# Performance work log

Measured on AMD Instinct MI355X. Metric: run time of the kernel, lower is better.

Reference implementation:

```python
import jax, jax.numpy as jnp
import numpy as np

B, N, D, H = 2, 2048, 1024, 16
DH = D // H
MASK_VALUE = -1e7


def setup_inputs() -> dict:
    key = jax.random.key(0)
    ks = jax.random.split(key, 8)
    scale = 0.02
    return {
        "queries": jax.random.normal(ks[0], (B, N, D), dtype=jnp.float32),
        "keys": jax.random.normal(ks[1], (B, N, D), dtype=jnp.float32),
        "values": jax.random.normal(ks[2], (B, N, D), dtype=jnp.float32),
        "valid_len": jax.random.randint(ks[3], (B * H,), 1, N + 1, dtype=jnp.int32),
        "Wq": jax.random.normal(ks[4], (D, D), dtype=jnp.float32) * scale,
        "Wk": jax.random.normal(ks[5], (D, D), dtype=jnp.float32) * scale,
        "Wv": jax.random.normal(ks[6], (D, D), dtype=jnp.float32) * scale,
        "Wo": jax.random.normal(ks[7], (D, D), dtype=jnp.float32) * scale,
    }


def reference(queries, keys, values, valid_len, Wq, Wk, Wv, Wo):
    b, n, d = queries.shape
    h, dh = H, d // H

    def split_heads(x):  # (b, n, d) -> (b, h, n, dh)
        return x.reshape(b, n, h, dh).transpose(0, 2, 1, 3)

    q = split_heads(queries @ Wq)
    k = split_heads(keys @ Wk)
    v = split_heads(values @ Wv)

    # (b, h, nq, nk) full score tensor, as in the original naive bmm path
    scores = jnp.einsum("bhqd,bhkd->bhqk", q, k) / jnp.sqrt(jnp.float32(dh))

    # valid_len is 1-D of length b*h; repeat_interleave over queries means the
    # mask depends only on the key index: keep k < valid_len[bh]
    vl = valid_len.reshape(b, h, 1, 1)
    keep = jnp.arange(n)[None, None, None, :] < vl  # (b, h, 1, nk)
    scores = jnp.where(keep, scores, MASK_VALUE)

    attn = jax.nn.softmax(scores, axis=-1)
    heads = jnp.einsum("bhqk,bhkd->bhqd", attn, v)  # (b, h, n, dh)
    out = heads.transpose(0, 2, 1, 3).reshape(b, n, d) @ Wo
    return out
```

## Files before the change

### kernel.cpp

```cpp
#include <hip/hip_runtime.h>

#define B_ 2
#define N_ 2048
#define D_ 1024
#define H_ 16
#define DH_ 64
#define NITEMS 1024

typedef _Float16 half8 __attribute__((ext_vector_type(8)));
typedef _Float16 half4 __attribute__((ext_vector_type(4)));
typedef float f32x4 __attribute__((ext_vector_type(4)));

__device__ __forceinline__ void gl2lds16(const _Float16* g, _Float16* l) {
  __builtin_amdgcn_global_load_lds(
      (const __attribute__((address_space(1))) void*)g,
      (__attribute__((address_space(3))) void*)l, 16, 0, 0);
}

__global__ __launch_bounds__(256) void prep_kernel(
    const float* __restrict__ q, const float* __restrict__ k,
    const float* __restrict__ v, const float* __restrict__ Wq,
    const float* __restrict__ Wk, const float* __restrict__ Wv,
    const float* __restrict__ Wo, const int* __restrict__ vlen,
    _Float16* __restrict__ Xf, _Float16* __restrict__ WtAll,
    int* __restrict__ order) {
  __shared__ float tile[64][65];
  const int bid = blockIdx.x;
  if (bid < 6144) {
    int y = bid >> 11, x = bid & 2047;
    const float* s = (y == 0) ? q : (y == 1) ? k : v;
    _Float16* d = Xf + (size_t)y * ((size_t)B_ * N_ * D_);
    size_t idx = ((size_t)x * 256 + threadIdx.x) * 8;
    float4 a = *(const float4*)(s + idx);
    float4 b = *(const float4*)(s + idx + 4);
    half8 h;
    h[0] = (_Float16)a.x; h[1] = (_Float16)a.y; h[2] = (_Float16)a.z; h[3] = (_Float16)a.w;
    h[4] = (_Float16)b.x; h[5] = (_Float16)b.y; h[6] = (_Float16)b.z; h[7] = (_Float16)b.w;
    *(half8*)(d + idx) = h;
  } else if (bid < 6144 + 1024) {
    int idx = bid - 6144;
    int z = idx >> 8, rem = idx & 255, gy = rem >> 4, gx = rem & 15;
    const float* W = (z == 0) ? Wq : (z == 1) ? Wk : (z == 2) ? Wv : Wo;
    _Float16* Wt = WtAll + (size_t)z * D_ * D_;
    int k0 = gy * 64, n0 = gx * 64;
    int tr = threadIdx.x >> 4, tc = threadIdx.x & 15;
#pragma unroll
    for (int i = 0; i < 4; ++i) {
      int r = tr + i * 16;
      float4 va = *(const float4*)(W + (size_t)(k0 + r) * D_ + n0 + tc * 4);
      tile[r][tc * 4 + 0] = va.x; tile[r][tc * 4 + 1] = va.y;
      tile[r][tc * 4 + 2] = va.z; tile[r][tc * 4 + 3] = va.w;
    }
    __syncthreads();
#pragma unroll
    for (int i = 0; i < 4; ++i) {
      int r = tr + i * 16;
      half4 hv;
      hv[0] = (_Float16)tile[tc * 4 + 0][r];
      hv[1] = (_Float16)tile[tc * 4 + 1][r];
      hv[2] = (_Float16)tile[tc * 4 + 2][r];
      hv[3] = (_Float16)tile[tc * 4 + 3][r];
      *(half4*)(Wt + (size_t)(n0 + r) * D_ + k0 + tc * 4) = hv;
    }
  } else {
    int i = threadIdx.x;
    if (i < B_ * H_) {
      int vi = vlen[i], rank = 0;
      for (int j = 0; j < B_ * H_; ++j) {
        int vj = vlen[j];
        if (vj > vi || (vj == vi && j < i)) ++rank;
      }
      order[rank] = i;
    }
  }
}

#define BK 32

template <int NT, int MODE>
__global__ __launch_bounds__(256) void gemm_f16_kernel(
    const _Float16* __restrict__ Aall, const _Float16* __restrict__ Btall,
    _Float16* __restrict__ ChAll, float* __restrict__ Cf32) {
  constexpr int BN = NT * 32;
  constexpr int K = D_;
  __shared__ __attribute__((aligned(16))) _Float16 As[128 * BK];
  __shared__ __attribute__((aligned(16))) _Float16 Bs[BN * BK];
  const int z = blockIdx.z;
  const _Float16* A  = Aall  + (size_t)z * ((size_t)B_ * N_ * D_);
  const _Float16* Bt = Btall + (size_t)z * ((size_t)D_ * D_);
  _Float16* Chead = ChAll + (size_t)z * ((size_t)B_ * N_ * D_);

  const int tid = threadIdx.x;
  const int m0 = blockIdx.y * 128, n0 = blockIdx.x * BN;
  const int lane = tid & 63, w = tid >> 6;
  const int quad = lane >> 4, l15 = lane & 15;
  const int wm = (w >> 1) * 64, wn = (w & 1) * (BN / 2);
  const int swz = (quad ^ ((l15 >> 1) & 3)) * 8;
  f32x4 acc[4][NT] = {};

  for (int kt = 0; kt < K; kt += BK) {
    if (kt) __syncthreads();
#pragma unroll
    for (int p = 0; p < 2; ++p) {
      int c = p * 256 + tid;
      int row = c >> 2, pg = c & 3;
      int gl = pg ^ ((row >> 1) & 3);
      gl2lds16(A + (size_t)(m0 + row) * K + kt + gl * 8, &As[c * 8]);
    }
#pragma unroll
    for (int p = 0; p < NT / 2; ++p) {
      int c = p * 256 + tid;
      int row = c >> 2, pg = c & 3;
      int gl = pg ^ ((row >> 1) & 3);
      gl2lds16(Bt + (size_t)(n0 + row) * K + kt + gl * 8, &Bs[c * 8]);
    }
    __syncthreads();
    half8 af[4], bf[NT];
#pragma unroll
    for (int mt = 0; mt < 4; ++mt)
      af[mt] = *(const half8*)&As[(wm + mt * 16 + l15) * 32 + swz];
#pragma unroll
    for (int nt = 0; nt < NT; ++nt)
      bf[nt] = *(const half8*)&Bs[(wn + nt * 16 + l15) * 32 + swz];
#pragma unroll
    for (int mt = 0; mt < 4; ++mt)
#pragma unroll
      for (int nt = 0; nt < NT; ++nt)
        acc[mt][nt] = __builtin_amdgcn_mfma_f32_16x16x32_f16(
            af[mt], bf[nt], acc[mt][nt], 0, 0, 0);
  }

#pragma unroll
  for (int mt = 0; mt < 4; ++mt) {
    int mrow = m0 + wm + mt * 16 + quad * 4;
#pragma unroll
    for (int nt = 0; nt < NT; ++nt) {
      int jcol = n0 + wn + nt * 16 + l15;
      if (MODE == 0) {
        int b = mrow >> 11, n = mrow & (N_ - 1);
        int h = jcol >> 6, dh = jcol & (DH_ - 1);
        if (z == 2) {
          half4 o;
#pragma unroll
          for (int r = 0; r < 4; ++r) o[r] = (_Float16)acc[mt][nt][r];
          *(half4*)(ChAll + 2 * (size_t)B_ * N_ * D_ +
                    ((size_t)(b * H_ + h) * DH_ + dh) * N_ + n) = o;
        } else {
#pragma unroll
          for (int r = 0; r < 4; ++r)
            Chead[((((size_t)(b * H_ + h)) * N_ + n + r) * DH_) + dh] =
                (_Float16)acc[mt][nt][r];
        }
      } else {
#pragma unroll
        for (int r = 0; r < 4; ++r)
          Cf32[(size_t)(mrow + r) * D_ + jcol] = acc[mt][nt][r];
      }
    }
  }
}

__global__ __launch_bounds__(256, 4) void attn_kernel(
    const _Float16* __restrict__ Qh, const _Float16* __restrict__ Kh,
    const _Float16* __restrict__ VtG, const int* __restrict__ vlen,
    _Float16* __restrict__ Hd, const int* __restrict__ order) {
  __shared__ __attribute__((aligned(16))) _Float16 Ks[2][64 * 64];
  __shared__ __attribute__((aligned(16))) _Float16 Vt[2][64 * 64];
  const int tid = threadIdx.x, lane = tid & 63, w = tid >> 6;
  const int quad = lane >> 4, l15 = lane & 15;
  const int sw  = (quad ^ (l15 & 7)) * 8;
  const int sw2 = ((quad + 4) ^ (l15 & 7)) * 8;
  const float sc2 = 0.125f * 1.44269504088896f;
  const half4 ones = {(_Float16)1, (_Float16)1, (_Float16)1, (_Float16)1};

  const int bid = blockIdx.x;
  const int item = (bid & 3) * 256 + (bid >> 2);
  const int bh = order[item >> 5];
  const int q0 = (item & 31) * 64;
  const int b = bh >> 4, h = bh & (H_ - 1);
  const int vl = vlen[bh];
  const int KT = (vl + 63) >> 6;
  const _Float16* Qb = Qh  + (size_t)bh * N_ * DH_;
  const _Float16* Kb = Kh  + (size_t)bh * N_ * DH_;
  const _Float16* Vb = VtG + (size_t)bh * N_ * DH_;

  const half8 qb0 = *(const half8*)(Qb + (size_t)(q0 + w * 16 + l15) * DH_ + quad * 8);
  const half8 qb1 = *(const half8*)(Qb + (size_t)(q0 + w * 16 + l15) * DH_ + 32 + quad * 8);

  half8 kpre[2], vpre[2];
  auto prefetch = [&](int k0k) {
#pragma unroll
    for (int p = 0; p < 2; ++p) {
      int c = p * 256 + tid;
      int row = c >> 3, pg = c & 7;
      kpre[p] = *(const half8*)(Kb + (size_t)(k0k + row) * DH_ + (pg ^ (row & 7)) * 8);
      vpre[p] = *(const half8*)(Vb + (size_t)row * N_ + k0k + pg * 8);
    }
  };
  auto commit = [&](int buf) {
#pragma unroll
    for (int p = 0; p < 2; ++p) {
      int c = p * 256 + tid;
      int row = c >> 3, pg = c & 7;
      *(half8*)&Ks[buf][c * 8] = kpre[p];
      int j0 = (pg * 2) ^ (row & 15), j1 = (pg * 2 + 1) ^ (row & 15);
      half4 lo = {vpre[p][0], vpre[p][1], vpre[p][2], vpre[p][3]};
      half4 hi = {vpre[p][4], vpre[p][5], vpre[p][6], vpre[p][7]};
      *(half4*)&Vt[buf][row * 64 + j0 * 4] = lo;
      *(half4*)&Vt[buf][row * 64 + j1 * 4] = hi;
    }
  };

  prefetch(0);
  commit(0);
  if (KT > 1) prefetch(64);
  __syncthreads();

  f32x4 Oacc[4] = {};
  f32x4 lacc = {};

  for (int kt = 0; kt < KT; ++kt) {
    const int cur = kt & 1;
    if (kt + 1 < KT) commit(1 - cur);
    if (kt + 2 < KT) prefetch((kt + 2) * 64);

    f32x4 s[4];
#pragma unroll
    for (int nt = 0; nt < 4; ++nt) {
      int r = nt * 16 + l15;
      half8 ka0 = *(const half8*)&Ks[cur][r * 64 + sw];
      half8 ka1 = *(const half8*)&Ks[cur][r * 64 + sw2];
      f32x4 c = {};
      c = __builtin_amdgcn_mfma_f32_16x16x32_f16(ka0, qb0, c, 0, 0, 0);
      c = __builtin_amdgcn_mfma_f32_16x16x32_f16(ka1, qb1, c, 0, 0, 0);
      s[nt] = c;
    }
    const int k0k = kt * 64;
    half4 pf[4];
    if (k0k + 64 <= vl) {
#pragma unroll
      for (int nt = 0; nt < 4; ++nt)
#pragma unroll
        for (int r = 0; r < 4; ++r)
          pf[nt][r] = (_Float16)exp2f(s[nt][r] * sc2);
    } else {
#pragma unroll
      for (int nt = 0; nt < 4; ++nt) {
        int keyb = k0k + nt * 16 + quad * 4;
#pragma unroll
        for (int r = 0; r < 4; ++r) {
          float p = exp2f(s[nt][r] * sc2);
          pf[nt][r] = (keyb + r < vl) ? (_Float16)p : (_Float16)0.f;
        }
      }
    }
#pragma unroll
    for (int nt = 0; nt < 4; ++nt) {
      lacc = __builtin_amdgcn_mfma_f32_16x16x16f16(ones, pf[nt], lacc, 0, 0, 0);
#pragma unroll
      for (int dt = 0; dt < 4; ++dt) {
        int dh = dt * 16 + l15;
        half4 va = *(const half4*)&Vt[cur][dh * 64 + (((nt * 4 + quad) ^ l15) << 2)];
        Oacc[dt] = __builtin_amdgcn_mfma_f32_16x16x16f16(va, pf[nt], Oacc[dt], 0, 0, 0);
      }
    }
    asm volatile("s_waitcnt lgkmcnt(0)" ::: "memory");
    __builtin_amdgcn_s_barrier();
    __builtin_amdgcn_sched_barrier(0);
  }

  float inv_l = 1.0f / lacc[0];
  int q = q0 + w * 16 + l15;
  _Float16* out = Hd + ((size_t)(b * N_ + q)) * D_ + h * DH_;
#pragma unroll
  for (int dt = 0; dt < 4; ++dt) {
    half4 o;
#pragma unroll
    for (int r = 0; r < 4; ++r) o[r] = (_Float16)(Oacc[dt][r] * inv_l);
    *(half4*)(out + dt * 16 + quad * 4) = o;
  }
}

extern "C" void kernel_launch(void* const* d_in, const int* in_sizes, int n_in,
                              void* d_out, int out_size, void* d_ws, size_t ws_size,
                              hipStream_t stream) {
  const float* q  = (const float*)d_in[0];
  const float* k  = (const float*)d_in[1];
  const float* v  = (const float*)d_in[2];
  const int*   vl = (const int*)d_in[3];
  const float* Wq = (const float*)d_in[4];
  const float* Wk = (const float*)d_in[5];
  const float* Wv = (const float*)d_in[6];
  const float* Wo = (const float*)d_in[7];

  const size_t XSZ = (size_t)B_ * N_ * D_;
  const size_t WSZ = (size_t)D_ * D_;
  _Float16* ws = (_Float16*)d_ws;
  _Float16* Xf = ws;
  _Float16* Wt = Xf + 3 * XSZ;
  _Float16* Qh = Wt + 4 * WSZ;
  _Float16* Hd = Qh + 3 * XSZ;
  int* order = (int*)(Hd + XSZ);

  prep_kernel<<<dim3(6144 + 1024 + 1), 256, 0, stream>>>(
      q, k, v, Wq, Wk, Wv, Wo, vl, Xf, Wt, order);

  gemm_f16_kernel<4, 0><<<dim3(D_ / 128, 32, 3), 256, 0, stream>>>(
      Xf, Wt, Qh, nullptr);

  attn_kernel<<<dim3(NITEMS), 256, 0, stream>>>(
      Qh, Qh + XSZ, Qh + 2 * XSZ, vl, Hd, order);

  gemm_f16_kernel<2, 1><<<dim3(D_ / 64, 32, 1), 256, 0, stream>>>(
      Hd, Wt + 3 * WSZ, nullptr, (float*)d_out);
}
```

Measured before the change: 236.4 us.

## Split attention keys across warps with register-direct K/V loads and LDS reduction

Restructures the attention kernel so each of the four warps handles all 64 queries but only a quarter of the key strips, reading K and V fragments straight from global memory into registers with a one-strip register prefetch. This removes the shared-memory staging of K/V tiles and the per-iteration block barriers. Partial O and row sums are then reduced across warps through LDS. It costs four times the accumulator registers, hence the lower occupancy hint, and uncoalesced scalar output stores. Block-index swizzling is also dropped.

```diff
diff --git a/kernel.cpp b/kernel.cpp
--- a/kernel.cpp
+++ b/kernel.cpp
@@ -160,124 +160,137 @@
   }
 }
 
-__global__ __launch_bounds__(256, 4) void attn_kernel(
+__global__ __launch_bounds__(256, 2) void attn_kernel(
     const _Float16* __restrict__ Qh, const _Float16* __restrict__ Kh,
     const _Float16* __restrict__ VtG, const int* __restrict__ vlen,
     _Float16* __restrict__ Hd, const int* __restrict__ order) {
-  __shared__ __attribute__((aligned(16))) _Float16 Ks[2][64 * 64];
-  __shared__ __attribute__((aligned(16))) _Float16 Vt[2][64 * 64];
+  __shared__ float Opart[2][64 * 65];
+  __shared__ float Lpart[2][64];
   const int tid = threadIdx.x, lane = tid & 63, w = tid >> 6;
   const int quad = lane >> 4, l15 = lane & 15;
-  const int sw  = (quad ^ (l15 & 7)) * 8;
-  const int sw2 = ((quad + 4) ^ (l15 & 7)) * 8;
   const float sc2 = 0.125f * 1.44269504088896f;
   const half4 ones = {(_Float16)1, (_Float16)1, (_Float16)1, (_Float16)1};
 
-  const int bid = blockIdx.x;
-  const int item = (bid & 3) * 256 + (bid >> 2);
+  const int item = blockIdx.x;
   const int bh = order[item >> 5];
   const int q0 = (item & 31) * 64;
   const int b = bh >> 4, h = bh & (H_ - 1);
   const int vl = vlen[bh];
-  const int KT = (vl + 63) >> 6;
+
   const _Float16* Qb = Qh  + (size_t)bh * N_ * DH_;
   const _Float16* Kb = Kh  + (size_t)bh * N_ * DH_;
   const _Float16* Vb = VtG + (size_t)bh * N_ * DH_;
 
-  const half8 qb0 = *(const half8*)(Qb + (size_t)(q0 + w * 16 + l15) * DH_ + quad * 8);
-  const half8 qb1 = *(const half8*)(Qb + (size_t)(q0 + w * 16 + l15) * DH_ + 32 + quad * 8);
-
-  half8 kpre[2], vpre[2];
-  auto prefetch = [&](int k0k) {
-#pragma unroll
-    for (int p = 0; p < 2; ++p) {
-      int c = p * 256 + tid;
-      int row = c >> 3, pg = c & 7;
-      kpre[p] = *(const half8*)(Kb + (size_t)(k0k + row) * DH_ + (pg ^ (row & 7)) * 8);
-      vpre[p] = *(const half8*)(Vb + (size_t)row * N_ + k0k + pg * 8);
-    }
-  };
-  auto commit = [&](int buf) {
-#pragma unroll
-    for (int p = 0; p < 2; ++p) {
-      int c = p * 256 + tid;
-      int row = c >> 3, pg = c & 7;
-      *(half8*)&Ks[buf][c * 8] = kpre[p];
-      int j0 = (pg * 2) ^ (row & 15), j1 = (pg * 2 + 1) ^ (row & 15);
-      half4 lo = {vpre[p][0], vpre[p][1], vpre[p][2], vpre[p][3]};
-      half4 hi = {vpre[p][4], vpre[p][5], vpre[p][6], vpre[p][7]};
-      *(half4*)&Vt[buf][row * 64 + j0 * 4] = lo;
-      *(half4*)&Vt[buf][row * 64 + j1 * 4] = hi;
-    }
-  };
-
-  prefetch(0);
-  commit(0);
-  if (KT > 1) prefetch(64);
-  __syncthreads();
-
-  f32x4 Oacc[4] = {};
-  f32x4 lacc = {};
-
-  for (int kt = 0; kt < KT; ++kt) {
-    const int cur = kt & 1;
-    if (kt + 1 < KT) commit(1 - cur);
-    if (kt + 2 < KT) prefetch((kt + 2) * 64);
-
-    f32x4 s[4];
-#pragma unroll
-    for (int nt = 0; nt < 4; ++nt) {
-      int r = nt * 16 + l15;
-      half8 ka0 = *(const half8*)&Ks[cur][r * 64 + sw];
-      half8 ka1 = *(const half8*)&Ks[cur][r * 64 + sw2];
-      f32x4 c = {};
-      c = __builtin_amdgcn_mfma_f32_16x16x32_f16(ka0, qb0, c, 0, 0, 0);
-      c = __builtin_amdgcn_mfma_f32_16x16x32_f16(ka1, qb1, c, 0, 0, 0);
-      s[nt] = c;
-    }
-    const int k0k = kt * 64;
+  half8 qlo[4], qhi[4];
+#pragma unroll
+  for (int nt = 0; nt < 4; ++nt) {
+    const _Float16* qp = Qb + (size_t)(q0 + nt * 16 + l15) * DH_ + quad * 8;
+    qlo[nt] = *(const half8*)qp;
+    qhi[nt] = *(const half8*)(qp + 32);
+  }
+
+  f32x4 Oacc[4][4] = {};
+  f32x4 lacc[4] = {};
+
+  const int nstrip = (vl > 16 * w) ? ((vl - 16 * w + 63) >> 6) : 0;
+
+  const _Float16* kap = Kb + (size_t)(16 * w + l15) * DH_ + quad * 8;
+  const _Float16* vap = Vb + (size_t)l15 * N_ + 16 * w + quad * 4;
+
+  half8 kc0 = *(const half8*)kap;
+  half8 kc1 = *(const half8*)(kap + 32);
+  half4 vc0 = *(const half4*)vap;
+  half4 vc1 = *(const half4*)(vap + 16 * (size_t)N_);
+  half4 vc2 = *(const half4*)(vap + 32 * (size_t)N_);
+  half4 vc3 = *(const half4*)(vap + 48 * (size_t)N_);
+
+  for (int t = 0; t < nstrip; ++t) {
+    kap += 64 * DH_;
+    vap += 64;
+    half8 kn0 = *(const half8*)kap;
+    half8 kn1 = *(const half8*)(kap + 32);
+    half4 vn0 = *(const half4*)vap;
+    half4 vn1 = *(const half4*)(vap + 16 * (size_t)N_);
+    half4 vn2 = *(const half4*)(vap + 32 * (size_t)N_);
+    half4 vn3 = *(const half4*)(vap + 48 * (size_t)N_);
+
+    const int kbase = t * 64 + 16 * w;
     half4 pf[4];
-    if (k0k + 64 <= vl) {
-#pragma unroll
-      for (int nt = 0; nt < 4; ++nt)
-#pragma unroll
-        for (int r = 0; r < 4; ++r)
-          pf[nt][r] = (_Float16)exp2f(s[nt][r] * sc2);
+    if (kbase + 16 <= vl) {
+#pragma unroll
+      for (int nt = 0; nt < 4; ++nt) {
+        f32x4 c = {};
+        c = __builtin_amdgcn_mfma_f32_16x16x32_f16(kc0, qlo[nt], c, 0, 0, 0);
+        c = __builtin_amdgcn_mfma_f32_16x16x32_f16(kc1, qhi[nt], c, 0, 0, 0);
+#pragma unroll
+        for (int r = 0; r < 4; ++r) pf[nt][r] = (_Float16)exp2f(c[r] * sc2);
+      }
     } else {
+      const int keyb = kbase + quad * 4;
 #pragma unroll
       for (int nt = 0; nt < 4; ++nt) {
-        int keyb = k0k + nt * 16 + quad * 4;
+        f32x4 c = {};
+        c = __builtin_amdgcn_mfma_f32_16x16x32_f16(kc0, qlo[nt], c, 0, 0, 0);
+        c = __builtin_amdgcn_mfma_f32_16x16x32_f16(kc1, qhi[nt], c, 0, 0, 0);
 #pragma unroll
         for (int r = 0; r < 4; ++r) {
-          float p = exp2f(s[nt][r] * sc2);
+          float p = exp2f(c[r] * sc2);
           pf[nt][r] = (keyb + r < vl) ? (_Float16)p : (_Float16)0.f;
         }
       }
     }
 #pragma unroll
     for (int nt = 0; nt < 4; ++nt) {
-      lacc = __builtin_amdgcn_mfma_f32_16x16x16f16(ones, pf[nt], lacc, 0, 0, 0);
-#pragma unroll
-      for (int dt = 0; dt < 4; ++dt) {
-        int dh = dt * 16 + l15;
-        half4 va = *(const half4*)&Vt[cur][dh * 64 + (((nt * 4 + quad) ^ l15) << 2)];
-        Oacc[dt] = __builtin_amdgcn_mfma_f32_16x16x16f16(va, pf[nt], Oacc[dt], 0, 0, 0);
-      }
-    }
-    asm volatile("s_waitcnt lgkmcnt(0)" ::: "memory");
-    __builtin_amdgcn_s_barrier();
-    __builtin_amdgcn_sched_barrier(0);
-  }
-
-  float inv_l = 1.0f / lacc[0];
-  int q = q0 + w * 16 + l15;
-  _Float16* out = Hd + ((size_t)(b * N_ + q)) * D_ + h * DH_;
-#pragma unroll
-  for (int dt = 0; dt < 4; ++dt) {
-    half4 o;
-#pragma unroll
-    for (int r = 0; r < 4; ++r) o[r] = (_Float16)(Oacc[dt][r] * inv_l);
-    *(half4*)(out + dt * 16 + quad * 4) = o;
+      lacc[nt] = __builtin_amdgcn_mfma_f32_16x16x16f16(ones, pf[nt], lacc[nt], 0, 0, 0);
+      Oacc[0][nt] = __builtin_amdgcn_mfma_f32_16x16x16f16(vc0, pf[nt], Oacc[0][nt], 0, 0, 0);
+      Oacc[1][nt] = __builtin_amdgcn_mfma_f32_16x16x16f16(vc1, pf[nt], Oacc[1][nt], 0, 0, 0);
+      Oacc[2][nt] = __builtin_amdgcn_mfma_f32_16x16x16f16(vc2, pf[nt], Oacc[2][nt], 0, 0, 0);
+      Oacc[3][nt] = __builtin_amdgcn_mfma_f32_16x16x16f16(vc3, pf[nt], Oacc[3][nt], 0, 0, 0);
+    }
+    kc0 = kn0; kc1 = kn1;
+    vc0 = vn0; vc1 = vn1; vc2 = vn2; vc3 = vn3;
+  }
+
+  const int slot = w & 1;
+  if (w < 2) {
+#pragma unroll
+    for (int dt = 0; dt < 4; ++dt)
+#pragma unroll
+      for (int nt = 0; nt < 4; ++nt)
+#pragma unroll
+        for (int r = 0; r < 4; ++r)
+          Opart[slot][(dt * 16 + quad * 4 + r) * 65 + nt * 16 + l15] =
+              Oacc[dt][nt][r];
+    if (quad == 0)
+#pragma unroll
+      for (int nt = 0; nt < 4; ++nt)
+        Lpart[slot][nt * 16 + l15] = lacc[nt][0];
+  }
+  __syncthreads();
+  if (w >= 2) {
+#pragma unroll
+    for (int dt = 0; dt < 4; ++dt)
+#pragma unroll
+      for (int nt = 0; nt < 4; ++nt)
+#pragma unroll
+        for (int r = 0; r < 4; ++r)
+          Opart[slot][(dt * 16 + quad * 4 + r) * 65 + nt * 16 + l15] +=
+              Oacc[dt][nt][r];
+    if (quad == 0)
+#pragma unroll
+      for (int nt = 0; nt < 4; ++nt)
+        Lpart[slot][nt * 16 + l15] += lacc[nt][0];
+  }
+  __syncthreads();
+
+  const int dh = w * 16 + l15;
+#pragma unroll
+  for (int q4 = 0; q4 < 16; ++q4) {
+    int qq = q4 * 4 + quad;
+    float o = Opart[0][dh * 65 + qq] + Opart[1][dh * 65 + qq];
+    float l = Lpart[0][qq] + Lpart[1][qq];
+    float inv_l = 1.0f / l;
+    Hd[((size_t)(b * N_ + q0 + qq)) * D_ + h * DH_ + dh] = (_Float16)(o * inv_l);
   }
 }
 
```

Result: faster. 228.4 us (-3.4%).

## Read K and V tiles directly from global memory, dropping LDS staging

Applied to the files above, without the earlier changes.

The attention kernel no longer stages K and V tiles through double-buffered shared memory with a prefetch/commit scheme and per-tile barriers. Each wave now loads its MFMA operands straight from global memory, relying on L1/L2 caching, since all four waves read the same K/V tiles. The block-index swizzle that interleaved work items across blocks is also removed. This cuts LDS traffic and synchronisation, but every wave now issues redundant global loads, loses explicit software prefetch, and has more load latency exposed in the loop.

```diff
diff --git a/kernel.cpp b/kernel.cpp
--- a/kernel.cpp
+++ b/kernel.cpp
@@ -164,17 +164,12 @@
     const _Float16* __restrict__ Qh, const _Float16* __restrict__ Kh,
     const _Float16* __restrict__ VtG, const int* __restrict__ vlen,
     _Float16* __restrict__ Hd, const int* __restrict__ order) {
-  __shared__ __attribute__((aligned(16))) _Float16 Ks[2][64 * 64];
-  __shared__ __attribute__((aligned(16))) _Float16 Vt[2][64 * 64];
   const int tid = threadIdx.x, lane = tid & 63, w = tid >> 6;
   const int quad = lane >> 4, l15 = lane & 15;
-  const int sw  = (quad ^ (l15 & 7)) * 8;
-  const int sw2 = ((quad + 4) ^ (l15 & 7)) * 8;
   const float sc2 = 0.125f * 1.44269504088896f;
   const half4 ones = {(_Float16)1, (_Float16)1, (_Float16)1, (_Float16)1};
 
-  const int bid = blockIdx.x;
-  const int item = (bid & 3) * 256 + (bid >> 2);
+  const int item = blockIdx.x;
   const int bh = order[item >> 5];
   const int q0 = (item & 31) * 64;
   const int b = bh >> 4, h = bh & (H_ - 1);
@@ -187,55 +182,34 @@
   const half8 qb0 = *(const half8*)(Qb + (size_t)(q0 + w * 16 + l15) * DH_ + quad * 8);
   const half8 qb1 = *(const half8*)(Qb + (size_t)(q0 + w * 16 + l15) * DH_ + 32 + quad * 8);
 
-  half8 kpre[2], vpre[2];
-  auto prefetch = [&](int k0k) {
-#pragma unroll
-    for (int p = 0; p < 2; ++p) {
-      int c = p * 256 + tid;
-      int row = c >> 3, pg = c & 7;
-      kpre[p] = *(const half8*)(Kb + (size_t)(k0k + row) * DH_ + (pg ^ (row & 7)) * 8);
-      vpre[p] = *(const half8*)(Vb + (size_t)row * N_ + k0k + pg * 8);
-    }
-  };
-  auto commit = [&](int buf) {
-#pragma unroll
-    for (int p = 0; p < 2; ++p) {
-      int c = p * 256 + tid;
-      int row = c >> 3, pg = c & 7;
-      *(half8*)&Ks[buf][c * 8] = kpre[p];
-      int j0 = (pg * 2) ^ (row & 15), j1 = (pg * 2 + 1) ^ (row & 15);
-      half4 lo = {vpre[p][0], vpre[p][1], vpre[p][2], vpre[p][3]};
-      half4 hi = {vpre[p][4], vpre[p][5], vpre[p][6], vpre[p][7]};
-      *(half4*)&Vt[buf][row * 64 + j0 * 4] = lo;
-      *(half4*)&Vt[buf][row * 64 + j1 * 4] = hi;
-    }
-  };
-
-  prefetch(0);
-  commit(0);
-  if (KT > 1) prefetch(64);
-  __syncthreads();
+  const _Float16* krow = Kb + (size_t)l15 * DH_ + quad * 8;
+  const _Float16* vrow = Vb + (size_t)l15 * N_ + quad * 4;
 
   f32x4 Oacc[4] = {};
   f32x4 lacc = {};
 
   for (int kt = 0; kt < KT; ++kt) {
-    const int cur = kt & 1;
-    if (kt + 1 < KT) commit(1 - cur);
-    if (kt + 2 < KT) prefetch((kt + 2) * 64);
+    const int k0k = kt * 64;
+
+    half4 va[4][4];
+#pragma unroll
+    for (int dt = 0; dt < 4; ++dt)
+#pragma unroll
+      for (int nt = 0; nt < 4; ++nt)
+        va[dt][nt] = *(const half4*)(vrow + (size_t)dt * 16 * N_ + k0k + nt * 16);
 
     f32x4 s[4];
 #pragma unroll
     for (int nt = 0; nt < 4; ++nt) {
-      int r = nt * 16 + l15;
-      half8 ka0 = *(const half8*)&Ks[cur][r * 64 + sw];
-      half8 ka1 = *(const half8*)&Ks[cur][r * 64 + sw2];
+      const _Float16* kp = krow + (size_t)(k0k + nt * 16) * DH_;
+      half8 ka0 = *(const half8*)kp;
+      half8 ka1 = *(const half8*)(kp + 32);
       f32x4 c = {};
       c = __builtin_amdgcn_mfma_f32_16x16x32_f16(ka0, qb0, c, 0, 0, 0);
       c = __builtin_amdgcn_mfma_f32_16x16x32_f16(ka1, qb1, c, 0, 0, 0);
       s[nt] = c;
     }
-    const int k0k = kt * 64;
+
     half4 pf[4];
     if (k0k + 64 <= vl) {
 #pragma unroll
@@ -254,19 +228,14 @@
         }
       }
     }
+
 #pragma unroll
     for (int nt = 0; nt < 4; ++nt) {
       lacc = __builtin_amdgcn_mfma_f32_16x16x16f16(ones, pf[nt], lacc, 0, 0, 0);
 #pragma unroll
-      for (int dt = 0; dt < 4; ++dt) {
-        int dh = dt * 16 + l15;
-        half4 va = *(const half4*)&Vt[cur][dh * 64 + (((nt * 4 + quad) ^ l15) << 2)];
-        Oacc[dt] = __builtin_amdgcn_mfma_f32_16x16x16f16(va, pf[nt], Oacc[dt], 0, 0, 0);
-      }
-    }
-    asm volatile("s_waitcnt lgkmcnt(0)" ::: "memory");
-    __builtin_amdgcn_s_barrier();
-    __builtin_amdgcn_sched_barrier(0);
+      for (int dt = 0; dt < 4; ++dt)
+        Oacc[dt] = __builtin_amdgcn_mfma_f32_16x16x16f16(va[dt][nt], pf[nt], Oacc[dt], 0, 0, 0);
+    }
   }
 
   float inv_l = 1.0f / lacc[0];
```

Result: slower. 383.5 us (+62.2%).

## Double-buffer GEMM LDS tiles and simplify attention block ordering and barrier

Applied to the files above, without the earlier changes.

The projection GEMM now uses two LDS buffers and issues the global-to-LDS loads for the next K step before computing on the current one, so memory latency can overlap with MFMA work. There is now one barrier per step instead of two, at the cost of twice the shared memory. The attention kernel drops the interleaved block-to-item mapping in favour of a direct blockIdx mapping, which changes how heavy (long valid_len) items spread across CUs. It also replaces the manual lgkmcnt wait plus raw barrier with __syncthreads.

```diff
diff --git a/kernel.cpp b/kernel.cpp
--- a/kernel.cpp
+++ b/kernel.cpp
@@ -83,8 +83,9 @@
     _Float16* __restrict__ ChAll, float* __restrict__ Cf32) {
   constexpr int BN = NT * 32;
   constexpr int K = D_;
-  __shared__ __attribute__((aligned(16))) _Float16 As[128 * BK];
-  __shared__ __attribute__((aligned(16))) _Float16 Bs[BN * BK];
+  constexpr int NSTEP = K / BK;
+  __shared__ __attribute__((aligned(16))) _Float16 As[2][128 * BK];
+  __shared__ __attribute__((aligned(16))) _Float16 Bs[2][BN * BK];
   const int z = blockIdx.z;
   const _Float16* A  = Aall  + (size_t)z * ((size_t)B_ * N_ * D_);
   const _Float16* Bt = Btall + (size_t)z * ((size_t)D_ * D_);
@@ -98,36 +99,44 @@
   const int swz = (quad ^ ((l15 >> 1) & 3)) * 8;
   f32x4 acc[4][NT] = {};
 
-  for (int kt = 0; kt < K; kt += BK) {
-    if (kt) __syncthreads();
+  auto stage = [&](int buf, int kt) {
 #pragma unroll
     for (int p = 0; p < 2; ++p) {
       int c = p * 256 + tid;
       int row = c >> 2, pg = c & 3;
       int gl = pg ^ ((row >> 1) & 3);
-      gl2lds16(A + (size_t)(m0 + row) * K + kt + gl * 8, &As[c * 8]);
+      gl2lds16(A + (size_t)(m0 + row) * K + kt + gl * 8, &As[buf][c * 8]);
     }
 #pragma unroll
     for (int p = 0; p < NT / 2; ++p) {
       int c = p * 256 + tid;
       int row = c >> 2, pg = c & 3;
       int gl = pg ^ ((row >> 1) & 3);
-      gl2lds16(Bt + (size_t)(n0 + row) * K + kt + gl * 8, &Bs[c * 8]);
-    }
-    __syncthreads();
+      gl2lds16(Bt + (size_t)(n0 + row) * K + kt + gl * 8, &Bs[buf][c * 8]);
+    }
+  };
+
+  stage(0, 0);
+  __syncthreads();
+
+  int cur = 0;
+  for (int ks = 0; ks < NSTEP; ++ks) {
+    if (ks + 1 < NSTEP) stage(cur ^ 1, (ks + 1) * BK);
     half8 af[4], bf[NT];
 #pragma unroll
     for (int mt = 0; mt < 4; ++mt)
-      af[mt] = *(const half8*)&As[(wm + mt * 16 + l15) * 32 + swz];
+      af[mt] = *(const half8*)&As[cur][(wm + mt * 16 + l15) * 32 + swz];
 #pragma unroll
     for (int nt = 0; nt < NT; ++nt)
-      bf[nt] = *(const half8*)&Bs[(wn + nt * 16 + l15) * 32 + swz];
+      bf[nt] = *(const half8*)&Bs[cur][(wn + nt * 16 + l15) * 32 + swz];
 #pragma unroll
     for (int mt = 0; mt < 4; ++mt)
 #pragma unroll
       for (int nt = 0; nt < NT; ++nt)
         acc[mt][nt] = __builtin_amdgcn_mfma_f32_16x16x32_f16(
             af[mt], bf[nt], acc[mt][nt], 0, 0, 0);
+    __syncthreads();
+    cur ^= 1;
   }
 
 #pragma unroll
@@ -173,8 +182,7 @@
   const float sc2 = 0.125f * 1.44269504088896f;
   const half4 ones = {(_Float16)1, (_Float16)1, (_Float16)1, (_Float16)1};
 
-  const int bid = blockIdx.x;
-  const int item = (bid & 3) * 256 + (bid >> 2);
+  const int item = blockIdx.x;
   const int bh = order[item >> 5];
   const int q0 = (item & 31) * 64;
   const int b = bh >> 4, h = bh & (H_ - 1);
@@ -264,9 +272,7 @@
         Oacc[dt] = __builtin_amdgcn_mfma_f32_16x16x16f16(va, pf[nt], Oacc[dt], 0, 0, 0);
       }
     }
-    asm volatile("s_waitcnt lgkmcnt(0)" ::: "memory");
-    __builtin_amdgcn_s_barrier();
-    __builtin_amdgcn_sched_barrier(0);
+    __syncthreads();
   }
 
   float inv_l = 1.0f / lacc[0];
```

Result: faster. 220.9 us (-6.6%).
